# Optimization experiments

Hardware: AMD Instinct MI355X
Metric: run time of the kernel (lower is better)

## Reference

```python
import jax, jax.numpy as jnp
import numpy as np

NUM_EXPERTS = 8
D_MODEL = 1024
HIDDEN = 3 * D_MODEL
TOP_K = 2
LAMBDA = 0.01


def setup_inputs() -> dict:
    key = jax.random.key(0)
    k_x, k_w1, k_w2, k_r = jax.random.split(key, 4)
    B, T, C = 4, 2048, D_MODEL
    x = jax.random.normal(k_x, (B, T, C), dtype=jnp.float32)
    # per-expert SwishFFN weights (bias=False): W1 [E, C, H], W2 [E, H, C]
    W1 = jax.random.normal(k_w1, (NUM_EXPERTS, C, HIDDEN), dtype=jnp.float32) * (1.0 / np.sqrt(C))
    W2 = jax.random.normal(k_w2, (NUM_EXPERTS, HIDDEN, C), dtype=jnp.float32) * (1.0 / np.sqrt(HIDDEN))
    # router projection [C, E]
    Wr = jax.random.normal(k_r, (C, NUM_EXPERTS), dtype=jnp.float32) * (1.0 / np.sqrt(C))
    return {"x": x, "W1": W1, "W2": W2, "Wr": Wr}


def reference(x, W1, W2, Wr):
    B, T, C = x.shape
    E = W1.shape[0]
    xf = x.reshape(-1, C)                       # [N, C], N = B*T
    N = xf.shape[0]

    # Router: softmax over experts, keep top-k, renormalize among the k
    logits = xf @ Wr                            # [N, E]
    all_probs = jax.nn.softmax(logits, axis=-1)
    vals, idx = jax.lax.top_k(all_probs, TOP_K)  # [N, K]
    vals = vals / jnp.sum(vals, axis=-1, keepdims=True)
    routing_weight = jnp.zeros((N, E), dtype=xf.dtype).at[
        jnp.arange(N)[:, None], idx
    ].set(vals)                                  # sparse [N, E]

    # Expert combine: sum_e w_e * FFN_e(x); w_e == 0 for non-selected tokens,
    # so this equals the original masked gather/scatter loop exactly.
    out = jnp.zeros_like(xf)
    for e in range(E):
        h = jax.nn.silu(xf @ W1[e])              # [N, H]
        out = out + routing_weight[:, e:e + 1] * (h @ W2[e])

    # Load-balancing aux loss (fi detached)
    fi = jax.lax.stop_gradient(
        jnp.mean((routing_weight > 0).astype(xf.dtype), axis=0))
    pi = jnp.mean(all_probs, axis=0)
    aux_loss = LAMBDA * E * jnp.sum(fi * pi)

    return out.reshape(B, T, C), aux_loss
```

## Files before the change

kernel.cpp:

```cpp
#include <hip/hip_runtime.h>
#include <stdint.h>

#define N_TOK 8192
#define C_DIM 1024
#define H_DIM 3072
#define N_EXP 8
#define N_ASSIGN (N_TOK * 2)

typedef __attribute__((ext_vector_type(8))) short short8;
typedef __attribute__((ext_vector_type(4))) float f32x4;

__device__ __forceinline__ unsigned short f2bf(float f) {
    union { float f; uint32_t u; } v; v.f = f;
    uint32_t r = (v.u + 0x7FFFu + ((v.u >> 16) & 1u)) >> 16;
    return (unsigned short)r;
}

#define GLDS16(SRC, DST) __builtin_amdgcn_global_load_lds( \
    (const __attribute__((address_space(1))) void*)(SRC),  \
    (__attribute__((address_space(3))) void*)(DST), 16, 0, 0)

__global__ void transpose_bf16_kernel(const float* __restrict__ in, unsigned short* __restrict__ out,
                                      int rows, int cols) {
    __shared__ float tile[32][33];
    int e = blockIdx.z;
    const float* ip = in + (size_t)e * rows * cols;
    unsigned short* op = out + (size_t)e * rows * cols;
    int col0 = blockIdx.x * 32;
    int row0 = blockIdx.y * 32;
    int tx = threadIdx.x, ty = threadIdx.y;
    tile[ty][tx] = ip[(size_t)(row0 + ty) * cols + col0 + tx];
    __syncthreads();
    op[(size_t)(col0 + ty) * rows + row0 + tx] = f2bf(tile[tx][ty]);
}

__global__ __launch_bounds__(256) void router_kernel(const float* __restrict__ x, const float* __restrict__ Wr,
                                                     int2* __restrict__ idx2, float2* __restrict__ wgt2,
                                                     float* __restrict__ piAcc, int* __restrict__ cntAcc) {
    __shared__ float s_pi[8];
    __shared__ int s_cnt[8];
    int t = threadIdx.x;
    if (t < 8) { s_pi[t] = 0.f; s_cnt[t] = 0; }
    __syncthreads();
    int lane = t & 63;
    int wid = t >> 6;
    int gwv = blockIdx.x * 4 + wid;
    int nw = gridDim.x * 4;
    for (int n = gwv; n < N_TOK; n += nw) {
        float acc[8];
#pragma unroll
        for (int e = 0; e < 8; e++) acc[e] = 0.f;
        const float* xr = x + (size_t)n * C_DIM;
#pragma unroll
        for (int j = 0; j < 16; j++) {
            int k = lane + 64 * j;
            float xv = xr[k];
            const float4* wr4 = (const float4*)(Wr + (size_t)k * 8);
            float4 a = wr4[0], b = wr4[1];
            acc[0] += xv * a.x; acc[1] += xv * a.y; acc[2] += xv * a.z; acc[3] += xv * a.w;
            acc[4] += xv * b.x; acc[5] += xv * b.y; acc[6] += xv * b.z; acc[7] += xv * b.w;
        }
#pragma unroll
        for (int off = 1; off < 64; off <<= 1) {
#pragma unroll
            for (int e = 0; e < 8; e++) acc[e] += __shfl_xor(acc[e], off, 64);
        }
        float m = acc[0];
#pragma unroll
        for (int e = 1; e < 8; e++) m = fmaxf(m, acc[e]);
        float p[8]; float s = 0.f;
#pragma unroll
        for (int e = 0; e < 8; e++) { p[e] = __expf(acc[e] - m); s += p[e]; }
        float inv = 1.f / s;
#pragma unroll
        for (int e = 0; e < 8; e++) p[e] *= inv;
        int i0 = 0; float l0 = acc[0];
#pragma unroll
        for (int e = 1; e < 8; e++) if (acc[e] > l0) { l0 = acc[e]; i0 = e; }
        int i1 = -1; float l1 = -1e30f;
#pragma unroll
        for (int e = 0; e < 8; e++) if (e != i0 && acc[e] > l1) { l1 = acc[e]; i1 = e; }
        if (lane == 0) {
            float v0 = p[i0], v1 = p[i1];
            float rs = 1.f / (v0 + v1);
            idx2[n] = make_int2(i0, i1);
            wgt2[n] = make_float2(v0 * rs, v1 * rs);
            atomicAdd(&s_cnt[i0], 1);
            atomicAdd(&s_cnt[i1], 1);
#pragma unroll
            for (int e = 0; e < 8; e++) atomicAdd(&s_pi[e], p[e]);
        }
    }
    __syncthreads();
    if (t < 8) { atomicAdd(&piAcc[t], s_pi[t]); atomicAdd(&cntAcc[t], s_cnt[t]); }
}

__global__ void finalize_router_kernel(const int* __restrict__ cnt, const float* __restrict__ pi,
                                       int* __restrict__ off, float* __restrict__ aux_out) {
    if (threadIdx.x == 0) {
        int o = 0;
        float dot = 0.f;
        for (int e = 0; e < 8; e++) {
            off[e] = o;
            o += cnt[e];
            dot += (float)cnt[e] * pi[e];
        }
        aux_out[0] = 0.01f * 8.f * dot / ((float)N_TOK * (float)N_TOK);
    }
}

__global__ __launch_bounds__(256) void scatter_kernel(const int2* __restrict__ idx2, const float2* __restrict__ wgt2,
                                                      const int* __restrict__ off, int* __restrict__ cursor,
                                                      int* __restrict__ tok, float* __restrict__ gwArr) {
    __shared__ int lcnt[8], lbase[8];
    int t = threadIdx.x;
    if (t < 8) lcnt[t] = 0;
    __syncthreads();
    int a = blockIdx.x * 256 + t;
    int n = a >> 1, k = a & 1;
    int2 id = idx2[n];
    float2 w = wgt2[n];
    int e = k ? id.y : id.x;
    float wv = k ? w.y : w.x;
    int rank = atomicAdd(&lcnt[e], 1);
    __syncthreads();
    if (t < 8) lbase[t] = atomicAdd(&cursor[t], lcnt[t]);
    __syncthreads();
    int pos = off[e] + lbase[e] + rank;
    tok[pos] = n;
    gwArr[pos] = wv;
}

__global__ __launch_bounds__(256) void gather_kernel(const float* __restrict__ x, const int* __restrict__ tok,
                                                     unsigned short* __restrict__ xg) {
    int wid = threadIdx.x >> 6, lane = threadIdx.x & 63;
    int row = blockIdx.x * 4 + wid;
    int n = tok[row];
    const float4* src = (const float4*)(x + (size_t)n * C_DIM);
    ushort4* dst = (ushort4*)(xg + (size_t)row * C_DIM);
#pragma unroll
    for (int j = 0; j < 4; j++) {
        float4 v = src[lane + 64 * j];
        ushort4 o;
        o.x = f2bf(v.x); o.y = f2bf(v.y); o.z = f2bf(v.z); o.w = f2bf(v.w);
        dst[lane + 64 * j] = o;
    }
}

template <int EPI>
__global__ __launch_bounds__(256) void moe_gemm_kernel(
    const unsigned short* __restrict__ A, int ldA,
    const unsigned short* __restrict__ Bt, int ldB, int bRowOff, int bColOff,
    int K, int NY,
    const int* __restrict__ cnt, const int* __restrict__ off,
    const int* __restrict__ tok, const float* __restrict__ gwArr,
    unsigned short* __restrict__ hs, int ldH,
    float* __restrict__ out) {
    __shared__ unsigned short As[8192];
    __shared__ unsigned short Bs[8192];

    int nbs[8];
    int tot = 0;
#pragma unroll
    for (int i = 0; i < 8; i++) {
        nbs[i] = (cnt[i] + 127) >> 7;
        tot += nbs[i] * NY;
    }
    int p = blockIdx.x;
    int q = tot >> 3, r = tot & 7;
    int x = p & 7, s = p >> 3;
    int capx = (x < r) ? q + 1 : q;
    if (s >= capx) return;
    int wi = (x < r) ? x * (q + 1) + s : r * (q + 1) + (x - r) * q + s;

    int base = 0, e = -1, enb = 0, local = 0;
#pragma unroll
    for (int i = 0; i < 8; i++) {
        int sz = nbs[i] * NY;
        if (e < 0 && wi < base + sz) { e = i; enb = nbs[i]; local = wi - base; }
        base += sz;
    }
    if (e < 0) return;
    int y = local / enb;
    int mblk = local - y * enb;
    int M = cnt[e];
    int m0 = mblk * 128;
    int baseRow = off[e];
    int n0 = y * 128;

    int tid = threadIdx.x;
    int lane = tid & 63;
    int wid = tid >> 6;
    int wm = (wid >> 1) * 64;
    int wn = (wid & 1) * 64;

    f32x4 acc[4][4];
#pragma unroll
    for (int i = 0; i < 4; i++)
#pragma unroll
        for (int j = 0; j < 4; j++) acc[i][j] = (f32x4)0.f;

    const unsigned short* Bex = Bt + (size_t)e * (size_t)(C_DIM * H_DIM);

    const unsigned short* srcA[4];
    const unsigned short* srcB[4];
    int ldsOff[4];
#pragma unroll
    for (int i = 0; i < 4; i++) {
        int c = i * 256 + tid;
        int half = c >> 9;
        int w = c & 511;
        int line = w >> 3, cc = w & 7;
        int swz = cc ^ (line & 7);
        int row = (line << 1) | (swz >> 2);
        int kOff = half * 32 + (swz & 3) * 8;
        int rg = m0 + row; if (rg > M - 1) rg = M - 1;
        srcA[i] = A + (size_t)(baseRow + rg) * ldA + kOff;
        srcB[i] = Bex + (size_t)(bRowOff + n0 + row) * ldB + bColOff + kOff;
        ldsOff[i] = (c & ~63) * 8;
    }

    int kq = lane >> 4;
    int rsub = lane & 15;
    int offA[4], offB[4];
#pragma unroll
    for (int m = 0; m < 4; m++) {
        int rr = wm + m * 16 + rsub;
        int l = rr >> 1;
        int cidx = ((((rr & 1) << 2) | kq) ^ (l & 7));
        offA[m] = l * 64 + cidx * 8;
    }
#pragma unroll
    for (int n = 0; n < 4; n++) {
        int rr = wn + n * 16 + rsub;
        int l = rr >> 1;
        int cidx = ((((rr & 1) << 2) | kq) ^ (l & 7));
        offB[n] = l * 64 + cidx * 8;
    }

    int nt = K >> 6;
#pragma unroll 1
    for (int t = 0; t < nt; ++t) {
#pragma unroll
        for (int i = 0; i < 4; i++) {
            GLDS16(srcA[i], &As[ldsOff[i]]);
            GLDS16(srcB[i], &Bs[ldsOff[i]]);
            srcA[i] += 64; srcB[i] += 64;
        }
        __syncthreads();
#pragma unroll
        for (int kk = 0; kk < 2; kk++) {
            short8 a[4], b[4];
#pragma unroll
            for (int m = 0; m < 4; m++) a[m] = *(const short8*)&As[kk * 4096 + offA[m]];
#pragma unroll
            for (int n = 0; n < 4; n++) b[n] = *(const short8*)&Bs[kk * 4096 + offB[n]];
#pragma unroll
            for (int m = 0; m < 4; m++)
#pragma unroll
                for (int n = 0; n < 4; n++)
                    acc[m][n] = __builtin_amdgcn_mfma_f32_16x16x32_bf16(a[m], b[n], acc[m][n], 0, 0, 0);
        }
        __syncthreads();
    }

    int gRow = (lane >> 4) * 4;
    int cLane = lane & 15;
#pragma unroll
    for (int m = 0; m < 4; m++) {
#pragma unroll
        for (int j = 0; j < 4; j++) {
            int rr = m0 + wm + m * 16 + gRow + j;
            if (rr < M) {
                if (EPI == 0) {
#pragma unroll
                    for (int n = 0; n < 4; n++) {
                        int c = n0 + wn + n * 16 + cLane;
                        float v = acc[m][n][j];
                        float sv = v / (1.f + __expf(-v));
                        hs[(size_t)(baseRow + rr) * ldH + c] = f2bf(sv);
                    }
                } else {
                    int token = tok[baseRow + rr];
                    float w = gwArr[baseRow + rr];
#pragma unroll
                    for (int n = 0; n < 4; n++) {
                        int c = n0 + wn + n * 16 + cLane;
                        atomicAdd(&out[(size_t)token * C_DIM + c], w * acc[m][n][j]);
                    }
                }
            }
        }
    }
}

extern "C" void kernel_launch(void* const* d_in, const int* in_sizes, int n_in,
                              void* d_out, int out_size, void* d_ws, size_t ws_size,
                              hipStream_t stream) {
    const float* x = (const float*)d_in[0];
    const float* W1 = (const float*)d_in[1];
    const float* W2 = (const float*)d_in[2];
    const float* Wr = (const float*)d_in[3];
    float* out = (float*)d_out;

    char* p = (char*)d_ws;
    auto alloc = [&](size_t bytes) {
        char* r = p;
        p += (bytes + 255) & ~(size_t)255;
        return r;
    };
    float* pi = (float*)alloc(8 * sizeof(float));
    int* cntA = (int*)alloc(8 * sizeof(int));
    int* cursor = (int*)alloc(8 * sizeof(int));
    int* offA = (int*)alloc(8 * sizeof(int));
    int2* idx2 = (int2*)alloc((size_t)N_TOK * sizeof(int2));
    float2* wgt2 = (float2*)alloc((size_t)N_TOK * sizeof(float2));
    int* tok = (int*)alloc((size_t)N_ASSIGN * sizeof(int));
    float* gwA = (float*)alloc((size_t)N_ASSIGN * sizeof(float));
    unsigned short* W1bT = (unsigned short*)alloc((size_t)N_EXP * C_DIM * H_DIM * 2);
    unsigned short* W2bT = (unsigned short*)alloc((size_t)N_EXP * C_DIM * H_DIM * 2);
    unsigned short* xg = (unsigned short*)alloc((size_t)N_ASSIGN * C_DIM * 2);
    size_t used = (size_t)(p - (char*)d_ws);
    size_t remain = ws_size > used ? ws_size - used : 0;
    int HC = H_DIM;
    while (HC > 384 && (size_t)N_ASSIGN * HC * 2 > remain) HC >>= 1;
    unsigned short* hs = (unsigned short*)p;

    hipMemsetAsync(d_ws, 0, 1024, stream);
    hipMemsetAsync(d_out, 0, (size_t)N_TOK * C_DIM * sizeof(float), stream);

    dim3 tb(32, 32, 1);
    transpose_bf16_kernel<<<dim3(H_DIM / 32, C_DIM / 32, N_EXP), tb, 0, stream>>>(W1, W1bT, C_DIM, H_DIM);
    transpose_bf16_kernel<<<dim3(C_DIM / 32, H_DIM / 32, N_EXP), tb, 0, stream>>>(W2, W2bT, H_DIM, C_DIM);

    router_kernel<<<256, 256, 0, stream>>>(x, Wr, idx2, wgt2, pi, cntA);
    finalize_router_kernel<<<1, 64, 0, stream>>>(cntA, pi, offA, out + (size_t)N_TOK * C_DIM);
    scatter_kernel<<<N_ASSIGN / 256, 256, 0, stream>>>(idx2, wgt2, offA, cursor, tok, gwA);
    gather_kernel<<<N_ASSIGN / 4, 256, 0, stream>>>(x, tok, xg);

    int nChunks = H_DIM / HC;
    for (int ci = 0; ci < nChunks; ++ci) {
        int h0 = ci * HC;
        int ny1 = HC / 128;
        moe_gemm_kernel<0><<<dim3(135 * ny1 + 8, 1, 1), 256, 0, stream>>>(
            xg, C_DIM, W1bT, C_DIM, h0, 0, C_DIM, ny1, cntA, offA, tok, gwA, hs, HC, out);
        moe_gemm_kernel<1><<<dim3(135 * 8 + 8, 1, 1), 256, 0, stream>>>(
            hs, HC, W2bT, H_DIM, 0, h0, HC, 8, cntA, offA, tok, gwA, hs, HC, out);
    }
}
```

Baseline: 499.3 us.

## Use 256x256 tiles with triple-buffered async LDS pipeline and split-K down projection

```diff
diff --git a/kernel.cpp b/kernel.cpp
--- a/kernel.cpp
+++ b/kernel.cpp
@@ -19,6 +19,14 @@
 #define GLDS16(SRC, DST) __builtin_amdgcn_global_load_lds( \
     (const __attribute__((address_space(1))) void*)(SRC),  \
     (__attribute__((address_space(3))) void*)(DST), 16, 0, 0)
+
+#define SBAR() do { __builtin_amdgcn_sched_barrier(0); \
+    __builtin_amdgcn_s_barrier();                      \
+    __builtin_amdgcn_sched_barrier(0); } while (0)
+
+#define VM_WAIT(S) do { __builtin_amdgcn_sched_barrier(0); \
+    asm volatile(S ::: "memory");                          \
+    __builtin_amdgcn_sched_barrier(0); } while (0)
 
 __global__ void transpose_bf16_kernel(const float* __restrict__ in, unsigned short* __restrict__ out,
                                       int rows, int cols) {
@@ -148,134 +156,171 @@
 }
 
 template <int EPI>
-__global__ __launch_bounds__(256) void moe_gemm_kernel(
+__global__ __launch_bounds__(512, 2) void moe_gemm_kernel(
     const unsigned short* __restrict__ A, int ldA,
     const unsigned short* __restrict__ Bt, int ldB, int bRowOff, int bColOff,
-    int K, int NY,
+    int Kseg, int NY, int SK,
     const int* __restrict__ cnt, const int* __restrict__ off,
     const int* __restrict__ tok, const float* __restrict__ gwArr,
     unsigned short* __restrict__ hs, int ldH,
     float* __restrict__ out) {
-    __shared__ unsigned short As[8192];
-    __shared__ unsigned short Bs[8192];
+    __shared__ unsigned short smem[49152];
 
     int nbs[8];
     int tot = 0;
 #pragma unroll
     for (int i = 0; i < 8; i++) {
-        nbs[i] = (cnt[i] + 127) >> 7;
-        tot += nbs[i] * NY;
+        nbs[i] = (cnt[i] + 255) >> 8;
+        tot += nbs[i] * NY * SK;
     }
     int p = blockIdx.x;
     int q = tot >> 3, r = tot & 7;
-    int x = p & 7, s = p >> 3;
-    int capx = (x < r) ? q + 1 : q;
-    if (s >= capx) return;
-    int wi = (x < r) ? x * (q + 1) + s : r * (q + 1) + (x - r) * q + s;
+    int xx = p & 7, sp = p >> 3;
+    int capx = (xx < r) ? q + 1 : q;
+    if (sp >= capx) return;
+    int wi = (xx < r) ? xx * (q + 1) + sp : r * (q + 1) + (xx - r) * q + sp;
 
     int base = 0, e = -1, enb = 0, local = 0;
 #pragma unroll
     for (int i = 0; i < 8; i++) {
-        int sz = nbs[i] * NY;
+        int sz = nbs[i] * NY * SK;
         if (e < 0 && wi < base + sz) { e = i; enb = nbs[i]; local = wi - base; }
         base += sz;
     }
     if (e < 0) return;
-    int y = local / enb;
-    int mblk = local - y * enb;
+    int ys = local / enb;
+    int mblk = local - ys * enb;
+    int s = ys / NY;
+    int y = ys - s * NY;
     int M = cnt[e];
-    int m0 = mblk * 128;
+    int m0 = mblk * 256;
     int baseRow = off[e];
-    int n0 = y * 128;
+    int n0 = y * 256;
+    int acol = s * Kseg;
+    int bcol = bColOff + s * Kseg;
 
     int tid = threadIdx.x;
     int lane = tid & 63;
     int wid = tid >> 6;
-    int wm = (wid >> 1) * 64;
-    int wn = (wid & 1) * 64;
-
-    f32x4 acc[4][4];
-#pragma unroll
-    for (int i = 0; i < 4; i++)
+    int wr = wid >> 2;
+    int wc = wid & 3;
+
+    f32x4 acc[8][4];
+#pragma unroll
+    for (int i = 0; i < 8; i++)
 #pragma unroll
         for (int j = 0; j < 4; j++) acc[i][j] = (f32x4)0.f;
 
     const unsigned short* Bex = Bt + (size_t)e * (size_t)(C_DIM * H_DIM);
 
-    const unsigned short* srcA[4];
-    const unsigned short* srcB[4];
-    int ldsOff[4];
-#pragma unroll
-    for (int i = 0; i < 4; i++) {
-        int c = i * 256 + tid;
-        int half = c >> 9;
-        int w = c & 511;
-        int line = w >> 3, cc = w & 7;
+    const unsigned short* srcA[2];
+    const unsigned short* srcB[2];
+    int ldsA[2], ldsB[2];
+    {
+        int c = tid;
+        int line = c >> 3, cc = c & 7;
         int swz = cc ^ (line & 7);
-        int row = (line << 1) | (swz >> 2);
-        int kOff = half * 32 + (swz & 3) * 8;
-        int rg = m0 + row; if (rg > M - 1) rg = M - 1;
-        srcA[i] = A + (size_t)(baseRow + rg) * ldA + kOff;
-        srcB[i] = Bex + (size_t)(bRowOff + n0 + row) * ldB + bColOff + kOff;
-        ldsOff[i] = (c & ~63) * 8;
+        int lrow = (line << 1) | (swz >> 2);
+        int kOff = (swz & 3) * 8;
+        int lb = (c & ~63) * 8;
+#pragma unroll
+        for (int h = 0; h < 2; h++) {
+            int rg = m0 + h * 128 + lrow; if (rg > M - 1) rg = M - 1;
+            srcA[h] = A + (size_t)(baseRow + rg) * ldA + acol + kOff;
+            srcB[h] = Bex + (size_t)(bRowOff + n0 + h * 128 + lrow) * ldB + bcol + kOff;
+            ldsA[h] = h * 4096 + lb;
+            ldsB[h] = 8192 + h * 4096 + lb;
+        }
     }
 
     int kq = lane >> 4;
     int rsub = lane & 15;
-    int offA[4], offB[4];
-#pragma unroll
-    for (int m = 0; m < 4; m++) {
-        int rr = wm + m * 16 + rsub;
-        int l = rr >> 1;
-        int cidx = ((((rr & 1) << 2) | kq) ^ (l & 7));
-        offA[m] = l * 64 + cidx * 8;
+    int offA[8], offB[4];
+#pragma unroll
+    for (int m = 0; m < 8; m++) {
+        int lr = m * 16 + rsub;
+        int l = lr >> 1;
+        int ch = ((((lr & 1) << 2) | kq) ^ (l & 7));
+        offA[m] = wr * 4096 + l * 64 + ch * 8;
     }
 #pragma unroll
     for (int n = 0; n < 4; n++) {
-        int rr = wn + n * 16 + rsub;
-        int l = rr >> 1;
-        int cidx = ((((rr & 1) << 2) | kq) ^ (l & 7));
-        offB[n] = l * 64 + cidx * 8;
-    }
-
-    int nt = K >> 6;
+        int lc = (wc & 1) * 64 + n * 16 + rsub;
+        int l = lc >> 1;
+        int ch = ((((lc & 1) << 2) | kq) ^ (l & 7));
+        offB[n] = 8192 + (wc >> 1) * 4096 + l * 64 + ch * 8;
+    }
+
+    int nt = Kseg >> 5;
+#pragma unroll
+    for (int h = 0; h < 2; h++) GLDS16(srcA[h], &smem[0 * 16384 + ldsA[h]]);
+#pragma unroll
+    for (int h = 0; h < 2; h++) GLDS16(srcB[h], &smem[0 * 16384 + ldsB[h]]);
+#pragma unroll
+    for (int h = 0; h < 2; h++) { srcA[h] += 32; GLDS16(srcA[h], &smem[1 * 16384 + ldsA[h]]); }
+#pragma unroll
+    for (int h = 0; h < 2; h++) { srcB[h] += 32; GLDS16(srcB[h], &smem[1 * 16384 + ldsB[h]]); }
+#pragma unroll
+    for (int h = 0; h < 2; h++) { srcA[h] += 32; srcB[h] += 32; }
+
+    int cur = 0, nb = 2;
 #pragma unroll 1
     for (int t = 0; t < nt; ++t) {
-#pragma unroll
-        for (int i = 0; i < 4; i++) {
-            GLDS16(srcA[i], &As[ldsOff[i]]);
-            GLDS16(srcB[i], &Bs[ldsOff[i]]);
-            srcA[i] += 64; srcB[i] += 64;
-        }
-        __syncthreads();
-#pragma unroll
-        for (int kk = 0; kk < 2; kk++) {
+        if (t == nt - 1) VM_WAIT("s_waitcnt vmcnt(0)");
+        else             VM_WAIT("s_waitcnt vmcnt(4)");
+        SBAR();
+        const unsigned short* buf = &smem[cur * 16384];
+        bool dostage = (t < nt - 2);
+        {
             short8 a[4], b[4];
 #pragma unroll
-            for (int m = 0; m < 4; m++) a[m] = *(const short8*)&As[kk * 4096 + offA[m]];
-#pragma unroll
-            for (int n = 0; n < 4; n++) b[n] = *(const short8*)&Bs[kk * 4096 + offB[n]];
+            for (int m = 0; m < 4; m++) a[m] = *(const short8*)&buf[offA[m]];
+#pragma unroll
+            for (int n = 0; n < 4; n++) b[n] = *(const short8*)&buf[offB[n]];
+            if (dostage) {
+                int bb = nb * 16384;
+#pragma unroll
+                for (int h = 0; h < 2; h++) { GLDS16(srcA[h], &smem[bb + ldsA[h]]); srcA[h] += 32; }
+            }
+            __builtin_amdgcn_s_setprio(1);
 #pragma unroll
             for (int m = 0; m < 4; m++)
 #pragma unroll
                 for (int n = 0; n < 4; n++)
                     acc[m][n] = __builtin_amdgcn_mfma_f32_16x16x32_bf16(a[m], b[n], acc[m][n], 0, 0, 0);
-        }
-        __syncthreads();
+            __builtin_amdgcn_s_setprio(0);
+            short8 a2[4];
+#pragma unroll
+            for (int m = 0; m < 4; m++) a2[m] = *(const short8*)&buf[offA[4 + m]];
+            if (dostage) {
+                int bb = nb * 16384;
+#pragma unroll
+                for (int h = 0; h < 2; h++) { GLDS16(srcB[h], &smem[bb + ldsB[h]]); srcB[h] += 32; }
+            }
+            __builtin_amdgcn_s_setprio(1);
+#pragma unroll
+            for (int m = 0; m < 4; m++)
+#pragma unroll
+                for (int n = 0; n < 4; n++)
+                    acc[4 + m][n] = __builtin_amdgcn_mfma_f32_16x16x32_bf16(a2[m], b[n], acc[4 + m][n], 0, 0, 0);
+            __builtin_amdgcn_s_setprio(0);
+        }
+        cur = (cur == 2) ? 0 : cur + 1;
+        nb = (nb == 2) ? 0 : nb + 1;
     }
 
     int gRow = (lane >> 4) * 4;
     int cLane = lane & 15;
 #pragma unroll
-    for (int m = 0; m < 4; m++) {
+    for (int m = 0; m < 8; m++) {
 #pragma unroll
         for (int j = 0; j < 4; j++) {
-            int rr = m0 + wm + m * 16 + gRow + j;
+            int rr = m0 + wr * 128 + m * 16 + gRow + j;
             if (rr < M) {
                 if (EPI == 0) {
 #pragma unroll
                     for (int n = 0; n < 4; n++) {
-                        int c = n0 + wn + n * 16 + cLane;
+                        int c = n0 + wc * 64 + n * 16 + cLane;
                         float v = acc[m][n][j];
                         float sv = v / (1.f + __expf(-v));
                         hs[(size_t)(baseRow + rr) * ldH + c] = f2bf(sv);
@@ -285,7 +330,7 @@
                     float w = gwArr[baseRow + rr];
 #pragma unroll
                     for (int n = 0; n < 4; n++) {
-                        int c = n0 + wn + n * 16 + cLane;
+                        int c = n0 + wc * 64 + n * 16 + cLane;
                         atomicAdd(&out[(size_t)token * C_DIM + c], w * acc[m][n][j]);
                     }
                 }
@@ -323,7 +368,7 @@
     size_t used = (size_t)(p - (char*)d_ws);
     size_t remain = ws_size > used ? ws_size - used : 0;
     int HC = H_DIM;
-    while (HC > 384 && (size_t)N_ASSIGN * HC * 2 > remain) HC >>= 1;
+    while (HC > 768 && (size_t)N_ASSIGN * HC * 2 > remain) HC >>= 1;
     unsigned short* hs = (unsigned short*)p;
 
     hipMemsetAsync(d_ws, 0, 1024, stream);
@@ -341,10 +386,13 @@
     int nChunks = H_DIM / HC;
     for (int ci = 0; ci < nChunks; ++ci) {
         int h0 = ci * HC;
-        int ny1 = HC / 128;
-        moe_gemm_kernel<0><<<dim3(135 * ny1 + 8, 1, 1), 256, 0, stream>>>(
-            xg, C_DIM, W1bT, C_DIM, h0, 0, C_DIM, ny1, cntA, offA, tok, gwA, hs, HC, out);
-        moe_gemm_kernel<1><<<dim3(135 * 8 + 8, 1, 1), 256, 0, stream>>>(
-            hs, HC, W2bT, H_DIM, 0, h0, HC, 8, cntA, offA, tok, gwA, hs, HC, out);
-    }
-}
+        int ny1 = HC / 256;
+        int sk2 = (HC == 3072) ? 2 : 1;
+        moe_gemm_kernel<0><<<dim3(71 * ny1 + 8, 1, 1), 512, 0, stream>>>(
+            xg, C_DIM, W1bT, C_DIM, h0, 0, C_DIM, ny1, 1,
+            cntA, offA, tok, gwA, hs, HC, out);
+        moe_gemm_kernel<1><<<dim3(71 * 4 * sk2 + 8, 1, 1), 512, 0, stream>>>(
+            hs, HC, W2bT, H_DIM, 0, h0, HC / sk2, 4, sk2,
+            cntA, offA, tok, gwA, hs, HC, out);
+    }
+}
```

Result: slower. 524.1 us (+5.0%).

## Add split-K to second expert GEMM, simplify LDS swizzle, vectorize weight transpose

Applied to the files above, without the earlier changes.

```diff
diff --git a/kernel.cpp b/kernel.cpp
--- a/kernel.cpp
+++ b/kernel.cpp
@@ -20,18 +20,37 @@
     (const __attribute__((address_space(1))) void*)(SRC),  \
     (__attribute__((address_space(3))) void*)(DST), 16, 0, 0)
 
-__global__ void transpose_bf16_kernel(const float* __restrict__ in, unsigned short* __restrict__ out,
-                                      int rows, int cols) {
-    __shared__ float tile[32][33];
+__global__ __launch_bounds__(256) void transpose_bf16_kernel(const float* __restrict__ in,
+                                                             unsigned short* __restrict__ out,
+                                                             int rows, int cols) {
+    __shared__ float tile[64][65];
     int e = blockIdx.z;
     const float* ip = in + (size_t)e * rows * cols;
     unsigned short* op = out + (size_t)e * rows * cols;
-    int col0 = blockIdx.x * 32;
-    int row0 = blockIdx.y * 32;
-    int tx = threadIdx.x, ty = threadIdx.y;
-    tile[ty][tx] = ip[(size_t)(row0 + ty) * cols + col0 + tx];
-    __syncthreads();
-    op[(size_t)(col0 + ty) * rows + row0 + tx] = f2bf(tile[tx][ty]);
+    int c0 = blockIdx.x * 64;
+    int r0 = blockIdx.y * 64;
+    int t = threadIdx.x;
+    int lr = t >> 4, lc4 = t & 15;
+#pragma unroll
+    for (int it = 0; it < 4; it++) {
+        int r = lr + it * 16;
+        float4 v = *(const float4*)&ip[(size_t)(r0 + r) * cols + c0 + lc4 * 4];
+        tile[lc4 * 4 + 0][r] = v.x;
+        tile[lc4 * 4 + 1][r] = v.y;
+        tile[lc4 * 4 + 2][r] = v.z;
+        tile[lc4 * 4 + 3][r] = v.w;
+    }
+    __syncthreads();
+#pragma unroll
+    for (int it = 0; it < 4; it++) {
+        int oc = lr + it * 16;
+        ushort4 o;
+        o.x = f2bf(tile[oc][lc4 * 4 + 0]);
+        o.y = f2bf(tile[oc][lc4 * 4 + 1]);
+        o.z = f2bf(tile[oc][lc4 * 4 + 2]);
+        o.w = f2bf(tile[oc][lc4 * 4 + 3]);
+        *(ushort4*)&op[(size_t)(c0 + oc) * rows + r0 + lc4 * 4] = o;
+    }
 }
 
 __global__ __launch_bounds__(256) void router_kernel(const float* __restrict__ x, const float* __restrict__ Wr,
@@ -151,7 +170,7 @@
 __global__ __launch_bounds__(256) void moe_gemm_kernel(
     const unsigned short* __restrict__ A, int ldA,
     const unsigned short* __restrict__ Bt, int ldB, int bRowOff, int bColOff,
-    int K, int NY,
+    int Kseg, int NY, int SK,
     const int* __restrict__ cnt, const int* __restrict__ off,
     const int* __restrict__ tok, const float* __restrict__ gwArr,
     unsigned short* __restrict__ hs, int ldH,
@@ -164,29 +183,33 @@
 #pragma unroll
     for (int i = 0; i < 8; i++) {
         nbs[i] = (cnt[i] + 127) >> 7;
-        tot += nbs[i] * NY;
+        tot += nbs[i] * NY * SK;
     }
     int p = blockIdx.x;
     int q = tot >> 3, r = tot & 7;
-    int x = p & 7, s = p >> 3;
-    int capx = (x < r) ? q + 1 : q;
-    if (s >= capx) return;
-    int wi = (x < r) ? x * (q + 1) + s : r * (q + 1) + (x - r) * q + s;
+    int xx = p & 7, sp = p >> 3;
+    int capx = (xx < r) ? q + 1 : q;
+    if (sp >= capx) return;
+    int wi = (xx < r) ? xx * (q + 1) + sp : r * (q + 1) + (xx - r) * q + sp;
 
     int base = 0, e = -1, enb = 0, local = 0;
 #pragma unroll
     for (int i = 0; i < 8; i++) {
-        int sz = nbs[i] * NY;
+        int sz = nbs[i] * NY * SK;
         if (e < 0 && wi < base + sz) { e = i; enb = nbs[i]; local = wi - base; }
         base += sz;
     }
     if (e < 0) return;
-    int y = local / enb;
-    int mblk = local - y * enb;
+    int ys = local / enb;
+    int mblk = local - ys * enb;
+    int s = ys / NY;
+    int y = ys - s * NY;
     int M = cnt[e];
     int m0 = mblk * 128;
     int baseRow = off[e];
     int n0 = y * 128;
+    int acol = s * Kseg;
+    int bcol = bColOff + s * Kseg;
 
     int tid = threadIdx.x;
     int lane = tid & 63;
@@ -208,37 +231,33 @@
 #pragma unroll
     for (int i = 0; i < 4; i++) {
         int c = i * 256 + tid;
-        int half = c >> 9;
-        int w = c & 511;
-        int line = w >> 3, cc = w & 7;
-        int swz = cc ^ (line & 7);
-        int row = (line << 1) | (swz >> 2);
-        int kOff = half * 32 + (swz & 3) * 8;
+        int row = c >> 3;
+        int pos = c & 7;
+        int sc = pos ^ (row & 7);
         int rg = m0 + row; if (rg > M - 1) rg = M - 1;
-        srcA[i] = A + (size_t)(baseRow + rg) * ldA + kOff;
-        srcB[i] = Bex + (size_t)(bRowOff + n0 + row) * ldB + bColOff + kOff;
+        srcA[i] = A + (size_t)(baseRow + rg) * ldA + acol + sc * 8;
+        srcB[i] = Bex + (size_t)(bRowOff + n0 + row) * ldB + bcol + sc * 8;
         ldsOff[i] = (c & ~63) * 8;
     }
 
     int kq = lane >> 4;
     int rsub = lane & 15;
-    int offA[4], offB[4];
-#pragma unroll
-    for (int m = 0; m < 4; m++) {
-        int rr = wm + m * 16 + rsub;
-        int l = rr >> 1;
-        int cidx = ((((rr & 1) << 2) | kq) ^ (l & 7));
-        offA[m] = l * 64 + cidx * 8;
-    }
-#pragma unroll
-    for (int n = 0; n < 4; n++) {
-        int rr = wn + n * 16 + rsub;
-        int l = rr >> 1;
-        int cidx = ((((rr & 1) << 2) | kq) ^ (l & 7));
-        offB[n] = l * 64 + cidx * 8;
-    }
-
-    int nt = K >> 6;
+    int offAr[2][4], offBr[2][4];
+#pragma unroll
+    for (int kk = 0; kk < 2; kk++) {
+#pragma unroll
+        for (int m = 0; m < 4; m++) {
+            int rr = wm + m * 16 + rsub;
+            offAr[kk][m] = rr * 64 + (((kk * 4 + kq) ^ (rr & 7)) * 8);
+        }
+#pragma unroll
+        for (int n = 0; n < 4; n++) {
+            int rn = wn + n * 16 + rsub;
+            offBr[kk][n] = rn * 64 + (((kk * 4 + kq) ^ (rn & 7)) * 8);
+        }
+    }
+
+    int nt = Kseg >> 6;
 #pragma unroll 1
     for (int t = 0; t < nt; ++t) {
 #pragma unroll
@@ -252,9 +271,9 @@
         for (int kk = 0; kk < 2; kk++) {
             short8 a[4], b[4];
 #pragma unroll
-            for (int m = 0; m < 4; m++) a[m] = *(const short8*)&As[kk * 4096 + offA[m]];
-#pragma unroll
-            for (int n = 0; n < 4; n++) b[n] = *(const short8*)&Bs[kk * 4096 + offB[n]];
+            for (int m = 0; m < 4; m++) a[m] = *(const short8*)&As[offAr[kk][m]];
+#pragma unroll
+            for (int n = 0; n < 4; n++) b[n] = *(const short8*)&Bs[offBr[kk][n]];
 #pragma unroll
             for (int m = 0; m < 4; m++)
 #pragma unroll
@@ -329,9 +348,8 @@
     hipMemsetAsync(d_ws, 0, 1024, stream);
     hipMemsetAsync(d_out, 0, (size_t)N_TOK * C_DIM * sizeof(float), stream);
 
-    dim3 tb(32, 32, 1);
-    transpose_bf16_kernel<<<dim3(H_DIM / 32, C_DIM / 32, N_EXP), tb, 0, stream>>>(W1, W1bT, C_DIM, H_DIM);
-    transpose_bf16_kernel<<<dim3(C_DIM / 32, H_DIM / 32, N_EXP), tb, 0, stream>>>(W2, W2bT, H_DIM, C_DIM);
+    transpose_bf16_kernel<<<dim3(H_DIM / 64, C_DIM / 64, N_EXP), 256, 0, stream>>>(W1, W1bT, C_DIM, H_DIM);
+    transpose_bf16_kernel<<<dim3(C_DIM / 64, H_DIM / 64, N_EXP), 256, 0, stream>>>(W2, W2bT, H_DIM, C_DIM);
 
     router_kernel<<<256, 256, 0, stream>>>(x, Wr, idx2, wgt2, pi, cntA);
     finalize_router_kernel<<<1, 64, 0, stream>>>(cntA, pi, offA, out + (size_t)N_TOK * C_DIM);
@@ -342,9 +360,12 @@
     for (int ci = 0; ci < nChunks; ++ci) {
         int h0 = ci * HC;
         int ny1 = HC / 128;
+        int sk2 = (HC >= 1536) ? 2 : 1;
         moe_gemm_kernel<0><<<dim3(135 * ny1 + 8, 1, 1), 256, 0, stream>>>(
-            xg, C_DIM, W1bT, C_DIM, h0, 0, C_DIM, ny1, cntA, offA, tok, gwA, hs, HC, out);
-        moe_gemm_kernel<1><<<dim3(135 * 8 + 8, 1, 1), 256, 0, stream>>>(
-            hs, HC, W2bT, H_DIM, 0, h0, HC, 8, cntA, offA, tok, gwA, hs, HC, out);
-    }
-}
+            xg, C_DIM, W1bT, C_DIM, h0, 0, C_DIM, ny1, 1,
+            cntA, offA, tok, gwA, hs, HC, out);
+        moe_gemm_kernel<1><<<dim3(135 * 8 * sk2 + 8, 1, 1), 256, 0, stream>>>(
+            hs, HC, W2bT, H_DIM, 0, h0, HC / sk2, 8, sk2,
+            cntA, offA, tok, gwA, hs, HC, out);
+    }
+}
```

Result: faster. 450.9 us (-9.7%).
